# Optimization experiments

Hardware: AMD Instinct MI355X
Metric: run time of the kernel (lower is better)

Reference implementation:

```python
import jax, jax.numpy as jnp
import numpy as np

EPS = 1e-3  # keras LayerNormalization default epsilon

def layer_norm(x, gamma, beta):
    mu = jnp.mean(x, axis=-1, keepdims=True)
    var = jnp.var(x, axis=-1, keepdims=True)
    return (x - mu) * jax.lax.rsqrt(var + EPS) * gamma + beta

def setup_inputs() -> dict:
    key = jax.random.key(0)
    ks = jax.random.split(key, 10)
    B, N, FD, AD, PD, DP = 4, 512, 256, 256, 128, 64
    s = lambda k, *sh: jax.random.normal(k, sh, dtype=jnp.float32)
    return {
        "F": s(ks[0], B, N, FD),
        "D": s(ks[1], B, N, N, DP),
        "Wq": s(ks[2], FD, AD) / np.sqrt(FD),
        "Wk": s(ks[3], FD, AD) / np.sqrt(FD),
        "Wv": s(ks[4], FD, AD) / np.sqrt(FD),
        "g_f": jnp.ones((FD,), jnp.float32),
        "b_f": jnp.zeros((FD,), jnp.float32),
        "g_p": jnp.ones((DP,), jnp.float32),
        "b_p": jnp.zeros((DP,), jnp.float32),
        "W_pt": s(ks[5], DP, PD) / np.sqrt(DP),
        "b_pt": jnp.zeros((PD,), jnp.float32),
        "W_ph": s(ks[6], PD, 1) / np.sqrt(PD),
    }

def reference(F, D, Wq, Wk, Wv, g_f, b_f, g_p, b_p, W_pt, b_pt, W_ph):
    # features path
    Fn = layer_norm(F, g_f, b_f)                       # [B,N,FD]
    Q = Fn @ Wq                                        # [B,N,AD]
    K = Fn @ Wk
    V = Fn @ Wv
    # pair-bias path: LN -> Dense(pairs_dim)+bias -> Dense(num_heads=1)
    Bn = layer_norm(D, g_p, b_p)                       # [B,N,N,DP]
    Bt = Bn @ W_pt + b_pt                              # [B,N,N,PD]
    bias = (Bt @ W_ph)[..., 0]                         # [B,N,N]
    scalar = 1.0 / jnp.sqrt(jnp.float32(Q.shape[-1]))
    A = jnp.einsum('bqd,bkd->bqk', Q, K) + bias        # QK^T + pair bias
    A = jax.nn.softmax(scalar * A, axis=-1)
    O = jnp.einsum('bqk,bkd->bqd', A, V)               # [B,N,AD]
    return jnp.sum(O, axis=-1)                         # [B,N]
```

## Files before the change

kernel.cpp:

```cpp
#include <hip/hip_runtime.h>
#include <hip/hip_bf16.h>
#include <cstddef>

#define OFF_GW    0
#define OFF_WV    64
#define OFF_SC    320
#define OFF_VSUM  384
#define OFF_Q     2432
#define OFF_K     526720

typedef float v4f __attribute__((ext_vector_type(4)));

__global__ __launch_bounds__(256) void k0_consts(
    const float* __restrict__ Wv, const float* __restrict__ g_p,
    const float* __restrict__ b_p, const float* __restrict__ W_pt,
    const float* __restrict__ b_pt, const float* __restrict__ W_ph,
    float* __restrict__ ws) {
  int t = threadIdx.x;
  if (blockIdx.x < 64) {
    int row = blockIdx.x * 4 + (t >> 6);
    int l = t & 63;
    float s = 0.f;
#pragma unroll
    for (int j = 0; j < 4; ++j) s += Wv[row * 256 + l + 64 * j];
    for (int m = 32; m >= 1; m >>= 1) s += __shfl_xor(s, m);
    if (l == 0) ws[OFF_WV + row] = s;
  } else {
    __shared__ float wc_s[64];
    __shared__ float wph_s[128];
    if (t < 128) wph_s[t] = W_ph[t];
    __syncthreads();
    int c = t >> 2, sub = t & 3;
    float wc = 0.f;
#pragma unroll
    for (int j = 0; j < 32; ++j)
      wc += W_pt[c * 128 + sub * 32 + j] * wph_s[sub * 32 + j];
    wc += __shfl_xor(wc, 1);
    wc += __shfl_xor(wc, 2);
    if (sub == 0) {
      wc_s[c] = wc;
      ws[OFF_GW + c] = g_p[c] * wc;
    }
    __syncthreads();
    if (t == 0) {
      float sg = 0.f, bc = 0.f;
      for (int cc = 0; cc < 64; ++cc) {
        sg += g_p[cc] * wc_s[cc];
        bc += b_p[cc] * wc_s[cc];
      }
      for (int p = 0; p < 128; ++p) bc += b_pt[p] * wph_s[p];
      ws[OFF_SC] = sg;
      ws[OFF_SC + 1] = bc;
    }
  }
}

__global__ __launch_bounds__(256) void k1_ln_qk(
    const float* __restrict__ F, const float* __restrict__ Wq,
    const float* __restrict__ Wk, const float* __restrict__ g_f,
    const float* __restrict__ b_f, float* __restrict__ ws) {
  __shared__ __align__(16) float fn[8][260];
  __shared__ float smu[8], srn[8];
  int t = threadIdx.x;
  int g = blockIdx.x >> 1, h = blockIdx.x & 1;
  int row0 = g * 8;
  const float* Fp = F + (size_t)row0 * 256;
#pragma unroll
  for (int k = 0; k < 8; ++k) fn[k][t] = Fp[k * 256 + t];
  __syncthreads();
  int r = t >> 5, l32 = t & 31;
  float s1 = 0.f, s2 = 0.f;
#pragma unroll
  for (int m = 0; m < 8; ++m) {
    float x = fn[r][l32 + 32 * m];
    s1 += x;
    s2 += x * x;
  }
  for (int m = 16; m >= 1; m >>= 1) {
    s1 += __shfl_xor(s1, m);
    s2 += __shfl_xor(s2, m);
  }
  if (l32 == 0) {
    float mu = s1 * (1.f / 256.f);
    float var = s2 * (1.f / 256.f) - mu * mu;
    smu[r] = mu;
    srn[r] = rsqrtf(var + 1e-3f);
  }
  __syncthreads();
  float gf = g_f[t], bf = b_f[t];
#pragma unroll
  for (int k = 0; k < 8; ++k)
    fn[k][t] = (fn[k][t] - smu[k]) * srn[k] * gf + bf;
  __syncthreads();
  if (h == 0) {
    const float* wv = ws + OFF_WV;
    float s = 0.f;
#pragma unroll
    for (int m = 0; m < 8; ++m) s += fn[r][l32 + 32 * m] * wv[l32 + 32 * m];
    for (int m = 16; m >= 1; m >>= 1) s += __shfl_xor(s, m);
    if (l32 == 0) ws[OFF_VSUM + row0 + r] = s;
  }
  int matsel = t >> 7;
  int col = h * 128 + (t & 127);
  const float* W = matsel ? Wk : Wq;
  float acc[8] = {0, 0, 0, 0, 0, 0, 0, 0};
#pragma unroll 2
  for (int f = 0; f < 256; f += 4) {
    float w0 = W[(f + 0) * 256 + col];
    float w1 = W[(f + 1) * 256 + col];
    float w2 = W[(f + 2) * 256 + col];
    float w3 = W[(f + 3) * 256 + col];
#pragma unroll
    for (int k = 0; k < 8; ++k) {
      v4f x = *(const v4f*)(&fn[k][f]);
      acc[k] = fmaf(x.w, w3,
               fmaf(x.z, w2, fmaf(x.y, w1, fmaf(x.x, w0, acc[k]))));
    }
  }
  float* Out = ws + (matsel ? OFF_K : OFF_Q) + (size_t)row0 * 256 + col;
#pragma unroll
  for (int k = 0; k < 8; ++k) Out[k * 256] = acc[k];
}

__global__ __launch_bounds__(256) void kb_bias_attn(
    const float* __restrict__ D, const float* __restrict__ ws,
    float* __restrict__ out) {
  __shared__ float4 Qs4[4][64];
  __shared__ float Sx[4][512];
  __shared__ float vs[512];
  int t = threadIdx.x;
  int b = blockIdx.x >> 7;
  int tile = blockIdx.x & 127;
  int q0 = tile * 4;
  int rowbase = b * 512 + q0;
  float* qsf = (float*)Qs4;
#pragma unroll
  for (int k = 0; k < 4; ++k)
    qsf[k * 256 + t] = ws[OFF_Q + (size_t)(rowbase + k) * 256 + t];
  vs[t] = ws[OFF_VSUM + b * 512 + t];
  vs[t + 256] = ws[OFF_VSUM + b * 512 + 256 + t];
  float sum_gw = ws[OFF_SC];
  float bconst = ws[OFF_SC + 1];
  int qq = t & 3;
  float4 g[4];
#pragma unroll
  for (int j = 0; j < 4; ++j) g[j] = ((const float4*)(ws + OFF_GW))[qq * 4 + j];

  int e4 = t >> 2;
  const float* Dbase = D + (size_t)rowbase * 512 * 64;
#pragma unroll 4
  for (int pi = 0; pi < 32; ++pi) {
    int rr = pi >> 3;
    int kk = (pi & 7) * 64 + e4;
    const v4f* dp =
        (const v4f*)(Dbase + ((size_t)rr * 512 + kk) * 64 + qq * 16);
    float s1 = 0.f, s2 = 0.f, sw = 0.f;
#pragma unroll
    for (int j = 0; j < 4; ++j) {
      v4f x = __builtin_nontemporal_load(dp + j);
      s1 += x.x + x.y + x.z + x.w;
      s2 += x.x * x.x + x.y * x.y + x.z * x.z + x.w * x.w;
      sw += x.x * g[j].x + x.y * g[j].y + x.z * g[j].z + x.w * g[j].w;
    }
    s1 += __shfl_xor(s1, 1);
    s2 += __shfl_xor(s2, 1);
    sw += __shfl_xor(sw, 1);
    s1 += __shfl_xor(s1, 2);
    s2 += __shfl_xor(s2, 2);
    sw += __shfl_xor(sw, 2);
    if (qq == 0) {
      float mu = s1 * (1.f / 64.f);
      float var = s2 * (1.f / 64.f) - mu * mu;
      float rn = rsqrtf(var + 1e-3f);
      Sx[rr][kk] = (rn * (sw - mu * sum_gw) + bconst) * 0.0625f;
    }
  }
  __syncthreads();

  const float* Kg = ws + OFF_K;
  const float4* K0p = (const float4*)(Kg + (size_t)(b * 512 + t) * 256);
  const float4* K1p = (const float4*)(Kg + (size_t)(b * 512 + 256 + t) * 256);
  float a0[4] = {0, 0, 0, 0}, a1[4] = {0, 0, 0, 0};
#pragma unroll 4
  for (int f = 0; f < 64; ++f) {
    float4 kv0 = K0p[f];
    float4 kv1 = K1p[f];
#pragma unroll
    for (int rr = 0; rr < 4; ++rr) {
      float4 qv = Qs4[rr][f];
      a0[rr] += qv.x * kv0.x + qv.y * kv0.y + qv.z * kv0.z + qv.w * kv0.w;
      a1[rr] += qv.x * kv1.x + qv.y * kv1.y + qv.z * kv1.z + qv.w * kv1.w;
    }
  }
#pragma unroll
  for (int rr = 0; rr < 4; ++rr) {
    Sx[rr][t] += a0[rr] * 0.0625f;
    Sx[rr][t + 256] += a1[rr] * 0.0625f;
  }
  __syncthreads();

  int w = t >> 6, l = t & 63;
  float m = -1e30f;
#pragma unroll
  for (int j = 0; j < 8; ++j) m = fmaxf(m, Sx[w][l + 64 * j]);
  for (int mm = 32; mm >= 1; mm >>= 1) m = fmaxf(m, __shfl_xor(m, mm));
  float se = 0.f, sv = 0.f;
#pragma unroll
  for (int j = 0; j < 8; ++j) {
    float ev = __expf(Sx[w][l + 64 * j] - m);
    se += ev;
    sv += ev * vs[l + 64 * j];
  }
  for (int mm = 32; mm >= 1; mm >>= 1) {
    se += __shfl_xor(se, mm);
    sv += __shfl_xor(sv, mm);
  }
  if (l == 0) out[rowbase + w] = sv / se;
}

extern "C" void kernel_launch(void* const* d_in, const int* in_sizes, int n_in,
                              void* d_out, int out_size, void* d_ws,
                              size_t ws_size, hipStream_t stream) {
  const float* F    = (const float*)d_in[0];
  const float* D    = (const float*)d_in[1];
  const float* Wq   = (const float*)d_in[2];
  const float* Wk   = (const float*)d_in[3];
  const float* Wv   = (const float*)d_in[4];
  const float* g_f  = (const float*)d_in[5];
  const float* b_f  = (const float*)d_in[6];
  const float* g_p  = (const float*)d_in[7];
  const float* b_p  = (const float*)d_in[8];
  const float* W_pt = (const float*)d_in[9];
  const float* b_pt = (const float*)d_in[10];
  const float* W_ph = (const float*)d_in[11];
  float* out = (float*)d_out;
  float* ws = (float*)d_ws;

  k0_consts<<<65, 256, 0, stream>>>(Wv, g_p, b_p, W_pt, b_pt, W_ph, ws);
  k1_ln_qk<<<512, 256, 0, stream>>>(F, Wq, Wk, g_f, b_f, ws);
  kb_bias_attn<<<512, 256, 0, stream>>>(D, ws, out);
}
```

Baseline: 441.9 us.

## Stream pair tensor through LDS with double-buffered async global_load_lds

The pair-bias stage now has each wave handle one query row and stream its slice of D into a per-wave double-buffered LDS stage using global_load_lds, waiting on vmcnt so the next chunk loads while the current one is reduced. LDS reads use a rotated chunk order with matching rotated gamma weights to avoid bank conflicts. The Q·K loop unroll goes from 4 to 8. This targets latency hiding on the dominant D read, in exchange for extra LDS traffic and reliance on hand-written waitcnt encodings.

```diff
diff --git a/kernel.cpp b/kernel.cpp
--- a/kernel.cpp
+++ b/kernel.cpp
@@ -1,6 +1,6 @@
 #include <hip/hip_runtime.h>
-#include <hip/hip_bf16.h>
 #include <cstddef>
+#include <cstdint>
 
 #define OFF_GW    0
 #define OFF_WV    64
@@ -10,6 +10,12 @@
 #define OFF_K     526720
 
 typedef float v4f __attribute__((ext_vector_type(4)));
+
+__device__ __forceinline__ void load_lds_16B(const float* g, float* l) {
+  __builtin_amdgcn_global_load_lds(
+      (const __attribute__((address_space(1))) uint32_t*)g,
+      (__attribute__((address_space(3))) uint32_t*)l, 16, 0, 0);
+}
 
 __global__ __launch_bounds__(256) void k0_consts(
     const float* __restrict__ Wv, const float* __restrict__ g_p,
@@ -125,42 +131,60 @@
 __global__ __launch_bounds__(256) void kb_bias_attn(
     const float* __restrict__ D, const float* __restrict__ ws,
     float* __restrict__ out) {
-  __shared__ float4 Qs4[4][64];
+  __shared__ __align__(16) float stage[4][2][1024];
   __shared__ float Sx[4][512];
+  __shared__ __align__(16) float Qs[4][256];
   __shared__ float vs[512];
   int t = threadIdx.x;
-  int b = blockIdx.x >> 7;
-  int tile = blockIdx.x & 127;
-  int q0 = tile * 4;
-  int rowbase = b * 512 + q0;
-  float* qsf = (float*)Qs4;
+  int w = t >> 6, l = t & 63;
+  int b = blockIdx.x >> 7, tile = blockIdx.x & 127;
+  int rowbase = b * 512 + tile * 4;
+
 #pragma unroll
   for (int k = 0; k < 4; ++k)
-    qsf[k * 256 + t] = ws[OFF_Q + (size_t)(rowbase + k) * 256 + t];
+    Qs[k][t] = ws[OFF_Q + (size_t)(rowbase + k) * 256 + t];
   vs[t] = ws[OFF_VSUM + b * 512 + t];
   vs[t + 256] = ws[OFF_VSUM + b * 512 + 256 + t];
   float sum_gw = ws[OFF_SC];
   float bconst = ws[OFF_SC + 1];
-  int qq = t & 3;
-  float4 g[4];
-#pragma unroll
-  for (int j = 0; j < 4; ++j) g[j] = ((const float4*)(ws + OFF_GW))[qq * 4 + j];
-
-  int e4 = t >> 2;
-  const float* Dbase = D + (size_t)rowbase * 512 * 64;
-#pragma unroll 4
-  for (int pi = 0; pi < 32; ++pi) {
-    int rr = pi >> 3;
-    int kk = (pi & 7) * 64 + e4;
-    const v4f* dp =
-        (const v4f*)(Dbase + ((size_t)rr * 512 + kk) * 64 + qq * 16);
+  int qq = l & 3, e4 = l >> 2;
+  v4f g_rot[4];
+#pragma unroll
+  for (int j = 0; j < 4; ++j) {
+    int p = (e4 + j) & 3;
+    g_rot[j] = *(const v4f*)(ws + OFF_GW + qq * 16 + p * 4);
+  }
+  __syncthreads();
+
+  const float* Dw = D + (size_t)(rowbase + w) * 512 * 64;
+  float* buf0 = &stage[w][0][0];
+  float* buf1 = &stage[w][1][0];
+#pragma unroll
+  for (int j = 0; j < 4; ++j)
+    load_lds_16B(Dw + j * 256 + l * 4, buf0 + j * 256);
+
+  for (int i = 0; i < 32; ++i) {
+    float* cur = (i & 1) ? buf1 : buf0;
+    float* nxt = (i & 1) ? buf0 : buf1;
+    if (i + 1 < 32) {
+#pragma unroll
+      for (int j = 0; j < 4; ++j)
+        load_lds_16B(Dw + (i + 1) * 1024 + j * 256 + l * 4, nxt + j * 256);
+      __builtin_amdgcn_s_waitcnt(0x0F74);
+    } else {
+      __builtin_amdgcn_s_waitcnt(0x0F70);
+    }
+    asm volatile("" ::: "memory");
+    const float* ebase = cur + e4 * 64 + qq * 16;
     float s1 = 0.f, s2 = 0.f, sw = 0.f;
 #pragma unroll
     for (int j = 0; j < 4; ++j) {
-      v4f x = __builtin_nontemporal_load(dp + j);
+      int p = (e4 + j) & 3;
+      v4f x = *(const v4f*)(ebase + p * 4);
       s1 += x.x + x.y + x.z + x.w;
       s2 += x.x * x.x + x.y * x.y + x.z * x.z + x.w * x.w;
-      sw += x.x * g[j].x + x.y * g[j].y + x.z * g[j].z + x.w * g[j].w;
+      sw += x.x * g_rot[j].x + x.y * g_rot[j].y + x.z * g_rot[j].z +
+            x.w * g_rot[j].w;
     }
     s1 += __shfl_xor(s1, 1);
     s2 += __shfl_xor(s2, 1);
@@ -172,22 +196,22 @@
       float mu = s1 * (1.f / 64.f);
       float var = s2 * (1.f / 64.f) - mu * mu;
       float rn = rsqrtf(var + 1e-3f);
-      Sx[rr][kk] = (rn * (sw - mu * sum_gw) + bconst) * 0.0625f;
+      Sx[w][i * 16 + e4] = (rn * (sw - mu * sum_gw) + bconst) * 0.0625f;
     }
   }
   __syncthreads();
 
   const float* Kg = ws + OFF_K;
-  const float4* K0p = (const float4*)(Kg + (size_t)(b * 512 + t) * 256);
-  const float4* K1p = (const float4*)(Kg + (size_t)(b * 512 + 256 + t) * 256);
+  const v4f* K0p = (const v4f*)(Kg + (size_t)(b * 512 + t) * 256);
+  const v4f* K1p = (const v4f*)(Kg + (size_t)(b * 512 + 256 + t) * 256);
   float a0[4] = {0, 0, 0, 0}, a1[4] = {0, 0, 0, 0};
-#pragma unroll 4
+#pragma unroll 8
   for (int f = 0; f < 64; ++f) {
-    float4 kv0 = K0p[f];
-    float4 kv1 = K1p[f];
+    v4f kv0 = K0p[f];
+    v4f kv1 = K1p[f];
 #pragma unroll
     for (int rr = 0; rr < 4; ++rr) {
-      float4 qv = Qs4[rr][f];
+      v4f qv = *(const v4f*)(&Qs[rr][f * 4]);
       a0[rr] += qv.x * kv0.x + qv.y * kv0.y + qv.z * kv0.z + qv.w * kv0.w;
       a1[rr] += qv.x * kv1.x + qv.y * kv1.y + qv.z * kv1.z + qv.w * kv1.w;
     }
@@ -199,7 +223,6 @@
   }
   __syncthreads();
 
-  int w = t >> 6, l = t & 63;
   float m = -1e30f;
 #pragma unroll
   for (int j = 0; j < 8; ++j) m = fmaxf(m, Sx[w][l + 64 * j]);
```

Measured after the change: 439.0 us. Within noise of the previous version (-0.7%).
